# Kernel tuning notes

Hardware: AMD Instinct MI355X
Metric: run time of the kernel (lower is better)

## Reference

```python
import jax, jax.numpy as jnp
import numpy as np

N_USERS = 100000
N_ITEMS = 50000
N_ENT = 80000            # items + tags (tags = 30000)
N_NODES = N_USERS + N_ENT
N_EDGES = 800000
D = 64
N_LAYERS = 2


def _center_net(embs, idx, n, W1, b1, W2, b2):
    # CenterIntersection: linear+relu, linear, segment softmax, weighted segment sum
    act = jnp.maximum(embs @ W1.T + b1, 0.0)
    logits = act @ W2.T + b2
    m = jax.ops.segment_max(logits, idx, num_segments=n)
    e = jnp.exp(logits - m[idx])
    s = jax.ops.segment_sum(e, idx, num_segments=n)
    att = e / s[idx]
    return jax.ops.segment_sum(att * embs, idx, num_segments=n)


def _offset_net(embs, idx, mask, n, use_min, W1, b1, W2, b2):
    # BoxOffsetIntersection restricted to edges where mask is True
    mf = mask[:, None].astype(embs.dtype)
    act = jnp.maximum(embs @ W1.T + b1, 0.0) * mf
    cnt = jax.ops.segment_sum(mask.astype(embs.dtype), idx, num_segments=n)
    mean = jax.ops.segment_sum(act, idx, num_segments=n) / jnp.maximum(cnt, 1.0)[:, None]
    gate = jax.nn.sigmoid(mean @ W2.T + b2)
    if use_min:
        src = jnp.where(mask[:, None], embs, jnp.inf)
        red = jax.ops.segment_min(src, idx, num_segments=n)
    else:
        src = jnp.where(mask[:, None], embs, -jnp.inf)
        red = jax.ops.segment_max(src, idx, num_segments=n)
    red = jnp.where(jnp.isfinite(red), red, 0.0)  # torch_scatter fills empty segments with 0
    return red * gate


def setup_inputs() -> dict:
    key = jax.random.key(0)
    ks = jax.random.split(key, 10)
    s = 0.05  # xavier-like scale
    return {
        "user_emb": jax.random.normal(ks[0], (N_USERS, D), jnp.float32),
        "user_offset_emb": jax.random.normal(ks[1], (N_USERS, D), jnp.float32),
        "item_emb": jax.random.normal(ks[2], (N_ENT, D), jnp.float32),
        "item_offset_emb": jax.random.normal(ks[3], (N_ENT, D), jnp.float32),
        "cW1": jax.random.normal(ks[4], (D, D), jnp.float32) * s,
        "cb1": jnp.zeros((D,), jnp.float32),
        "cW2": jax.random.normal(ks[5], (D, D), jnp.float32) * s,
        "cb2": jnp.zeros((D,), jnp.float32),
        "oW1": jax.random.normal(ks[6], (D, D), jnp.float32) * s,
        "ob1": jnp.zeros((D,), jnp.float32),
        "oW2": jax.random.normal(ks[7], (D, D), jnp.float32) * s,
        "ob2": jnp.zeros((D,), jnp.float32),
        "head": jax.random.randint(ks[8], (N_EDGES,), 0, N_NODES, jnp.int32),
        "tail": jax.random.randint(ks[9], (N_EDGES,), 0, N_NODES, jnp.int32),
    }


def reference(user_emb, user_offset_emb, item_emb, item_offset_emb,
              cW1, cb1, cW2, cb2, oW1, ob1, oW2, ob2, head, tail):
    all_embs = jnp.concatenate([user_emb, item_emb], axis=0)              # [N_NODES, D]
    all_off = jnp.maximum(jnp.concatenate([user_offset_emb, item_offset_emb], axis=0), 0.0)
    uu_idx = jnp.concatenate([jnp.arange(N_USERS), jnp.arange(N_USERS)])
    uu_mask = jnp.ones((2 * N_USERS,), bool)
    m_inter = (tail >= N_USERS) & (head < N_USERS) & (tail < N_USERS + N_ITEMS)
    m_ut = (head < N_USERS) & (tail >= N_USERS + N_ITEMS)
    m_item = (head >= N_USERS) & (head < N_USERS + N_ITEMS)
    m_tag = head >= N_USERS + N_ITEMS
    for _ in range(N_LAYERS):
        h_embs = all_embs[tail]                                           # [E, D] gather
        agg_emb = _center_net(h_embs, head, N_NODES, cW1, cb1, cW2, cb2)
        edge_off = jnp.maximum(all_off[tail], 0.0)                        # [E, D]
        inter_u = _offset_net(edge_off, head, m_inter, N_NODES, True, oW1, ob1, oW2, ob2)[:N_USERS]
        ut_u = _offset_net(edge_off, head, m_ut, N_NODES, False, oW1, ob1, oW2, ob2)[:N_USERS]
        item_o = _offset_net(edge_off, head, m_item, N_NODES, False, oW1, ob1, oW2, ob2)[N_USERS:N_USERS + N_ITEMS]
        tag_o = _offset_net(edge_off, head, m_tag, N_NODES, True, oW1, ob1, oW2, ob2)[N_USERS + N_ITEMS:]
        uo_cat = jnp.concatenate([inter_u, ut_u], axis=0)                 # [2*N_USERS, D]
        user_o = jnp.maximum(_offset_net(uo_cat, uu_idx, uu_mask, N_USERS, False, oW1, ob1, oW2, ob2), 0.0)
        agg_off = jnp.concatenate([user_o, item_o, tag_o], axis=0)
        agg_emb = agg_emb / jnp.maximum(jnp.linalg.norm(agg_emb, axis=1, keepdims=True), 1e-12)  # F.normalize
        all_embs = agg_emb
        all_off = agg_off
    return (all_embs[:N_USERS], all_off[:N_USERS], all_embs[N_USERS:], all_off[N_USERS:])
```

## Files before the change

### kernel.cpp

```cpp
#include <hip/hip_runtime.h>
#include <hip/hip_fp16.h>
#include <math.h>

#define NU 100000
#define NI 50000
#define NENT 80000
#define NN 180000
#define NEDGE 800000
#define SCAN_NB ((NN + 1023) / 1024)
#define UFIN_BLKS ((NU + 63) / 64)
#define EFIN_BLKS (NENT / 64)

typedef _Float16 f16x4 __attribute__((ext_vector_type(4)));
typedef _Float16 f16x2 __attribute__((ext_vector_type(2)));
typedef float f32x4 __attribute__((ext_vector_type(4)));

__device__ __forceinline__ float sigmoid_f(float x) { return 1.0f / (1.0f + __expf(-x)); }
__device__ __forceinline__ unsigned pack2(float a, float b) {
    __half2 h = __floats2half2_rn(a, b);
    return *(unsigned*)&h;
}
__device__ __forceinline__ f16x2 u2h2(unsigned u) { union { unsigned u; f16x2 h; } x; x.u = u; return x.h; }
__device__ __forceinline__ float fdot2f(f16x2 a, f16x2 b, float c) {
#if __has_builtin(__builtin_amdgcn_fdot2)
    return __builtin_amdgcn_fdot2(a, b, c, false);
#else
    return (float)a[0] * (float)b[0] + (float)a[1] * (float)b[1] + c;
#endif
}
__device__ __forceinline__ _Float16 hminf(_Float16 a, _Float16 b) { return a < b ? a : b; }
__device__ __forceinline__ _Float16 hmaxf(_Float16 a, _Float16 b) { return a > b ? a : b; }

template<typename T>
__device__ __forceinline__ f16x4 ldfrag(const T* __restrict__ p) {
    if constexpr (sizeof(T) == 2) {
        return *(const f16x4*)p;
    } else {
        float4 v = *(const float4*)p;
        f16x4 r; r[0] = (_Float16)v.x; r[1] = (_Float16)v.y; r[2] = (_Float16)v.z; r[3] = (_Float16)v.w;
        return r;
    }
}
template<typename T>
__device__ __forceinline__ f16x4 ldfragr(const T* __restrict__ p) {
    if constexpr (sizeof(T) == 2) {
        f16x4 v = *(const f16x4*)p;
        #pragma unroll
        for (int i = 0; i < 4; ++i) v[i] = hmaxf(v[i], (_Float16)0.f);
        return v;
    } else {
        float4 v = *(const float4*)p;
        f16x4 r;
        r[0] = (_Float16)fmaxf(v.x, 0.f); r[1] = (_Float16)fmaxf(v.y, 0.f);
        r[2] = (_Float16)fmaxf(v.z, 0.f); r[3] = (_Float16)fmaxf(v.w, 0.f);
        return r;
    }
}
__device__ __forceinline__ f16x4 fragp(const _Float16* __restrict__ Wp, int dt, int ks, int lane) {
    return *(const f16x4*)(Wp + (((dt * 4 + ks) * 64 + lane) << 2));
}
__device__ __forceinline__ f32x4 mm(f16x4 a, f16x4 b, f32x4 c) {
    return __builtin_amdgcn_mfma_f32_16x16x16f16(a, b, c, 0, 0, 0);
}

__global__ __launch_bounds__(256) void prep_w(
    const float* __restrict__ W0, const float* __restrict__ W1,
    const float* __restrict__ W2, const float* __restrict__ W3,
    _Float16* __restrict__ out)
{
    int idx = blockIdx.x * 256 + threadIdx.x;
    int mat = idx >> 12, wi = idx & 4095;
    const float* W = (mat == 0) ? W0 : (mat == 1) ? W1 : (mat == 2) ? W2 : W3;
    int tile = wi >> 8;
    int dt = tile >> 2, ks = tile & 3;
    int ln = (wi >> 2) & 63, j = wi & 3;
    int lr = ln & 15, lk = ln >> 4;
    out[idx] = (_Float16)W[(size_t)(dt * 16 + lr) * 64 + ks * 16 + lk * 4 + j];
}

template<typename T>
__global__ __launch_bounds__(256) void node_pass(
    const T* __restrict__ embU, const T* __restrict__ embE,
    const T* __restrict__ offU, const T* __restrict__ offE,
    const _Float16* __restrict__ cW1f, const float* __restrict__ cb1,
    const _Float16* __restrict__ cW2f, const float* __restrict__ cb2,
    const _Float16* __restrict__ oW1f, const float* __restrict__ ob1,
    unsigned* __restrict__ packedA, unsigned* __restrict__ packedB)
{
    __shared__ _Float16 tb[4][16 * 72];
    int lane = threadIdx.x & 63, wid = threadIdx.x >> 6;
    int n0 = (blockIdx.x * 4 + wid) * 16;
    if (n0 >= NN) return;
    int lr = lane & 15, lk = lane >> 4;
    const T* eb; const T* ob;
    if (n0 < NU) { eb = embU + (size_t)n0 * 64; ob = offU + (size_t)n0 * 64; }
    else         { eb = embE + (size_t)(n0 - NU) * 64; ob = offE + (size_t)(n0 - NU) * 64; }

    f16x4 ax[4];
    #pragma unroll
    for (int ks = 0; ks < 4; ++ks) ax[ks] = ldfrag(eb + (size_t)lr * 64 + ks * 16 + lk * 4);
    f32x4 acc[4];
    #pragma unroll
    for (int dt = 0; dt < 4; ++dt) {
        float b = cb1[dt * 16 + lr];
        f32x4 c = {b, b, b, b};
        #pragma unroll
        for (int ks = 0; ks < 4; ++ks) c = mm(ax[ks], fragp(cW1f, dt, ks, lane), c);
        acc[dt] = c;
    }
    _Float16* T16 = tb[wid];
    #pragma unroll
    for (int dt = 0; dt < 4; ++dt)
        #pragma unroll
        for (int r = 0; r < 4; ++r)
            T16[(lk * 4 + r) * 72 + dt * 16 + lr] = (_Float16)fmaxf(acc[dt][r], 0.f);
    f16x4 a1[4];
    #pragma unroll
    for (int ks = 0; ks < 4; ++ks) a1[ks] = *(const f16x4*)(T16 + lr * 72 + ks * 16 + lk * 4);
    #pragma unroll
    for (int dt = 0; dt < 4; ++dt) {
        float b = cb2[dt * 16 + lr];
        f32x4 c = {b, b, b, b};
        #pragma unroll
        for (int ks = 0; ks < 4; ++ks) c = mm(a1[ks], fragp(cW2f, dt, ks, lane), c);
        acc[dt] = c;
    }
    f16x4 axo[4];
    #pragma unroll
    for (int ks = 0; ks < 4; ++ks) axo[ks] = ldfragr(ob + (size_t)lr * 64 + ks * 16 + lk * 4);
    f32x4 acco[4];
    #pragma unroll
    for (int dt = 0; dt < 4; ++dt) {
        float b = ob1[dt * 16 + lr];
        f32x4 c = {b, b, b, b};
        #pragma unroll
        for (int ks = 0; ks < 4; ++ks) c = mm(axo[ks], fragp(oW1f, dt, ks, lane), c);
        acco[dt] = c;
    }
    #pragma unroll
    for (int ks = 0; ks < 4; ++ks) *(f16x4*)(T16 + lr * 72 + ks * 16 + lk * 4) = ax[ks];
    _Float16 xv[16];
    #pragma unroll
    for (int dt = 0; dt < 4; ++dt)
        #pragma unroll
        for (int r = 0; r < 4; ++r) xv[dt * 4 + r] = T16[(lk * 4 + r) * 72 + dt * 16 + lr];
    #pragma unroll
    for (int ks = 0; ks < 4; ++ks) *(f16x4*)(T16 + lr * 72 + ks * 16 + lk * 4) = axo[ks];
    #pragma unroll
    for (int dt = 0; dt < 4; ++dt) {
        #pragma unroll
        for (int r = 0; r < 4; ++r) {
            int li = lk * 4 + r;
            float ev = __expf(acc[dt][r]);
            float xf = (float)xv[dt * 4 + r];
            float ovf = (float)T16[(lk * 4 + r) * 72 + dt * 16 + lr];
            float aov = fmaxf(acco[dt][r], 0.f);
            size_t idx = (size_t)(n0 + li) * 64 + dt * 16 + lr;
            packedA[idx] = pack2(ev, ev * xf);
            packedB[idx] = pack2(aov, ovf);
        }
    }
}

__global__ __launch_bounds__(256) void hist_k(const int* __restrict__ head, int* __restrict__ counts) {
    int e = blockIdx.x * 256 + threadIdx.x;
    if (e < NEDGE) atomicAdd(&counts[head[e]], 1);
}

__global__ __launch_bounds__(1024) void scan_local(const int* __restrict__ counts,
                                                   int* __restrict__ excl, int* __restrict__ partials) {
    __shared__ int wsum[16];
    int tid = threadIdx.x, lane = tid & 63, wid = tid >> 6;
    int i = blockIdx.x * 1024 + tid;
    int v = (i < NN) ? counts[i] : 0;
    int s = v;
    #pragma unroll
    for (int d = 1; d < 64; d <<= 1) { int u = __shfl_up(s, d, 64); if (lane >= d) s += u; }
    if (lane == 63) wsum[wid] = s;
    __syncthreads();
    if (wid == 0 && lane < 16) {
        int w = wsum[lane];
        #pragma unroll
        for (int d = 1; d < 16; d <<= 1) { int u = __shfl_up(w, d, 64); if (lane >= d) w += u; }
        wsum[lane] = w;
    }
    __syncthreads();
    int base = wid ? wsum[wid - 1] : 0;
    if (i < NN) excl[i] = base + s - v;
    if (tid == 1023) partials[blockIdx.x] = wsum[15];
}

__global__ __launch_bounds__(256) void scan_carry(const int* __restrict__ partials, int* __restrict__ carries) {
    __shared__ int ws[4];
    int tid = threadIdx.x, lane = tid & 63, wid = tid >> 6;
    int v = (tid < SCAN_NB) ? partials[tid] : 0;
    int s = v;
    #pragma unroll
    for (int d = 1; d < 64; d <<= 1) { int u = __shfl_up(s, d, 64); if (lane >= d) s += u; }
    if (lane == 63) ws[wid] = s;
    __syncthreads();
    int add = 0;
    for (int w = 0; w < wid; ++w) add += ws[w];
    if (tid < SCAN_NB) carries[tid] = add + s - v;
}

__global__ __launch_bounds__(1024) void scan_add(int* __restrict__ excl, const int* __restrict__ carries,
                                                 int* __restrict__ cursor) {
    int i = blockIdx.x * 1024 + threadIdx.x;
    if (i < NN) { int o = excl[i] + carries[blockIdx.x]; excl[i] = o; cursor[i] = o; }
    if (i == 0) excl[NN] = NEDGE;
}

__global__ __launch_bounds__(256) void scatter_k(const int* __restrict__ head, const int* __restrict__ tail,
                                                 int* __restrict__ cursor, int* __restrict__ sorted_t) {
    int e = blockIdx.x * 256 + threadIdx.x;
    if (e < NEDGE) { int pos = atomicAdd(&cursor[head[e]], 1); sorted_t[pos] = tail[e]; }
}

template<bool OUT16>
__global__ __launch_bounds__(256) void seg_pass(
    const unsigned* __restrict__ packedA, const unsigned* __restrict__ packedB,
    const int* __restrict__ offsets, const int* __restrict__ sorted_t,
    void* __restrict__ embOutU_, void* __restrict__ embOutE_,
    _Float16* __restrict__ meanI, _Float16* __restrict__ redI,
    _Float16* __restrict__ meanU, _Float16* __restrict__ redU,
    _Float16* __restrict__ meanE, _Float16* __restrict__ redE)
{
    int lane = threadIdx.x & 63;
    int h = blockIdx.x * 4 + (threadIdx.x >> 6);
    int beg = offsets[h], end = offsets[h + 1];
    bool isUser = (h < NU);
    bool entMin = (h >= NU + NI);
    const f16x2 SEL_LO = {(_Float16)1.0f, (_Float16)0.0f};
    const f16x2 SEL_HI = {(_Float16)0.0f, (_Float16)1.0f};
    float num = 0.f, den = 0.f, s_i = 0.f, s_u = 0.f;
    const _Float16 HINF = u2h2(0x7C007C00u)[0];
    _Float16 m_i = (isUser || entMin) ? HINF : (_Float16)0.f;
    _Float16 m_u = (_Float16)0.f;
    int c_i = 0, c_u = 0;

    const char* pA = (const char*)packedA;
    const char* pB = (const char*)packedB;
    int loff = lane << 2;

#define LOADQ(t, a, b)                                                          \
    do {                                                                        \
        a = *(const unsigned*)(pA + ((size_t)(unsigned)(t) << 8) + loff);       \
        if (!isUser || (t) >= NU)                                               \
            b = *(const unsigned*)(pB + ((size_t)(unsigned)(t) << 8) + loff);   \
    } while (0)

#define CONSUME(tc, qa, qb)                                                     \
    do {                                                                        \
        f16x2 ea = u2h2(qa);                                                    \
        den = fdot2f(ea, SEL_LO, den);                                          \
        num = fdot2f(ea, SEL_HI, num);                                          \
        if (isUser) {                                                           \
            if ((tc) >= NU) {                                                   \
                f16x2 ab = u2h2(qb);                                            \
                if ((tc) < NU + NI) { s_i = fdot2f(ab, SEL_LO, s_i); m_i = hminf(m_i, ab[1]); c_i++; } \
                else                { s_u = fdot2f(ab, SEL_LO, s_u); m_u = hmaxf(m_u, ab[1]); c_u++; } \
            }                                                                   \
        } else {                                                                \
            f16x2 ab = u2h2(qb);                                                \
            s_i = fdot2f(ab, SEL_LO, s_i); c_i++;                               \
            m_i = entMin ? hminf(m_i, ab[1]) : hmaxf(m_i, ab[1]);               \
        }                                                                       \
    } while (0)

    for (int base = beg; base < end; base += 64) {
        int rem = end - base; if (rem > 64) rem = 64;
        int tv = sorted_t[base + (lane < rem ? lane : 0)];
        int tA = 0, tB = 0; unsigned aA = 0, aB = 0, bA = 0, bB = 0;
        tA = __builtin_amdgcn_readlane(tv, 0);
        LOADQ(tA, aA, bA);
        if (rem > 1) { tB = __builtin_amdgcn_readlane(tv, 1); LOADQ(tB, aB, bB); }
        int j = 0;
        for (; j + 2 <= rem; j += 2) {
            CONSUME(tA, aA, bA);
            if (j + 2 < rem) { tA = __builtin_amdgcn_readlane(tv, j + 2); LOADQ(tA, aA, bA); }
            CONSUME(tB, aB, bB);
            if (j + 3 < rem) { tB = __builtin_amdgcn_readlane(tv, j + 3); LOADQ(tB, aB, bB); }
        }
        if (j < rem) CONSUME(tA, aA, bA);
    }
#undef LOADQ
#undef CONSUME

    float v = (den > 0.f) ? num / den : 0.f;
    float sq = v * v;
    #pragma unroll
    for (int m = 32; m; m >>= 1) sq += __shfl_xor(sq, m, 64);
    v = v / fmaxf(sqrtf(sq), 1e-12f);

    float m_if = (float)m_i;
    if (m_if > 1e37f) m_if = 0.f;
    float rc_i = __builtin_amdgcn_rcpf(fmaxf((float)c_i, 1.f));
    if (isUser) {
        size_t r = (size_t)h * 64 + lane;
        if constexpr (OUT16) ((_Float16*)embOutU_)[r] = (_Float16)v;
        else                 ((float*)embOutU_)[r] = v;
        float rc_u = __builtin_amdgcn_rcpf(fmaxf((float)c_u, 1.f));
        meanI[r] = (_Float16)(s_i * rc_i);
        redI[r]  = (_Float16)m_if;
        meanU[r] = (_Float16)(s_u * rc_u);
        redU[r]  = m_u;
    } else {
        size_t r = (size_t)(h - NU) * 64 + lane;
        if constexpr (OUT16) ((_Float16*)embOutE_)[r] = (_Float16)v;
        else                 ((float*)embOutE_)[r] = v;
        meanE[r] = (_Float16)(s_i * rc_i);
        redE[r]  = (_Float16)m_if;
    }
}

template<bool OUT16>
__global__ __launch_bounds__(256) void fin_pass(
    const _Float16* __restrict__ meanI, const _Float16* __restrict__ redI,
    const _Float16* __restrict__ meanU, const _Float16* __restrict__ redU,
    const _Float16* __restrict__ meanE, const _Float16* __restrict__ redE,
    const _Float16* __restrict__ oW1f, const float* __restrict__ ob1,
    const _Float16* __restrict__ oW2f, const float* __restrict__ ob2,
    void* __restrict__ outOffU_, void* __restrict__ entOff_)
{
    int lane = threadIdx.x & 63, wid = threadIdx.x >> 6;
    int lr = lane & 15, lk = lane >> 4;

    if (blockIdx.x >= UFIN_BLKS) {
        int n0 = (((int)blockIdx.x - UFIN_BLKS) * 4 + wid) * 16;
        if (n0 >= NENT) return;
        f16x4 am[4];
        #pragma unroll
        for (int ks = 0; ks < 4; ++ks) am[ks] = *(const f16x4*)(meanE + (size_t)(n0 + lr) * 64 + ks * 16 + lk * 4);
        #pragma unroll
        for (int dt = 0; dt < 4; ++dt) {
            float b = ob2[dt * 16 + lr];
            f32x4 c = {b, b, b, b};
            #pragma unroll
            for (int ks = 0; ks < 4; ++ks) c = mm(am[ks], fragp(oW2f, dt, ks, lane), c);
            #pragma unroll
            for (int r = 0; r < 4; ++r) {
                size_t row = (size_t)(n0 + lk * 4 + r);
                float val = (float)redE[row * 64 + dt * 16 + lr] * sigmoid_f(c[r]);
                if constexpr (OUT16) ((_Float16*)entOff_)[row * 64 + dt * 16 + lr] = (_Float16)val;
                else                 ((float*)entOff_)[row * 64 + dt * 16 + lr] = val;
            }
        }
        return;
    }

    __shared__ _Float16 tb[4][16 * 72];
    int u0 = (blockIdx.x * 4 + wid) * 16;
    if (u0 >= NU) return;
    _Float16* T16 = tb[wid];

    f16x4 W1f[4][4], W2f[4][4];
    float b1d[4], b2d[4];
    #pragma unroll
    for (int dt = 0; dt < 4; ++dt) {
        b1d[dt] = ob1[dt * 16 + lr]; b2d[dt] = ob2[dt * 16 + lr];
        #pragma unroll
        for (int ks = 0; ks < 4; ++ks) {
            W1f[dt][ks] = fragp(oW1f, dt, ks, lane);
            W2f[dt][ks] = fragp(oW2f, dt, ks, lane);
        }
    }

    f16x4 am[4];
    #pragma unroll
    for (int ks = 0; ks < 4; ++ks) am[ks] = *(const f16x4*)(meanI + (size_t)(u0 + lr) * 64 + ks * 16 + lk * 4);
    f32x4 iu[4], uu[4];
    #pragma unroll
    for (int dt = 0; dt < 4; ++dt) {
        f32x4 c = {b2d[dt], b2d[dt], b2d[dt], b2d[dt]};
        #pragma unroll
        for (int ks = 0; ks < 4; ++ks) c = mm(am[ks], W2f[dt][ks], c);
        #pragma unroll
        for (int r = 0; r < 4; ++r)
            iu[dt][r] = (float)redI[(size_t)(u0 + lk * 4 + r) * 64 + dt * 16 + lr] * sigmoid_f(c[r]);
    }
    #pragma unroll
    for (int ks = 0; ks < 4; ++ks) am[ks] = *(const f16x4*)(meanU + (size_t)(u0 + lr) * 64 + ks * 16 + lk * 4);
    #pragma unroll
    for (int dt = 0; dt < 4; ++dt) {
        f32x4 c = {b2d[dt], b2d[dt], b2d[dt], b2d[dt]};
        #pragma unroll
        for (int ks = 0; ks < 4; ++ks) c = mm(am[ks], W2f[dt][ks], c);
        #pragma unroll
        for (int r = 0; r < 4; ++r)
            uu[dt][r] = (float)redU[(size_t)(u0 + lk * 4 + r) * 64 + dt * 16 + lr] * sigmoid_f(c[r]);
    }
    #pragma unroll
    for (int dt = 0; dt < 4; ++dt)
        #pragma unroll
        for (int r = 0; r < 4; ++r) T16[(lk * 4 + r) * 72 + dt * 16 + lr] = (_Float16)iu[dt][r];
    #pragma unroll
    for (int ks = 0; ks < 4; ++ks) am[ks] = *(const f16x4*)(T16 + lr * 72 + ks * 16 + lk * 4);
    f32x4 mn[4];
    #pragma unroll
    for (int dt = 0; dt < 4; ++dt) {
        f32x4 c = {b1d[dt], b1d[dt], b1d[dt], b1d[dt]};
        #pragma unroll
        for (int ks = 0; ks < 4; ++ks) c = mm(am[ks], W1f[dt][ks], c);
        #pragma unroll
        for (int r = 0; r < 4; ++r) mn[dt][r] = fmaxf(c[r], 0.f);
    }
    #pragma unroll
    for (int dt = 0; dt < 4; ++dt)
        #pragma unroll
        for (int r = 0; r < 4; ++r) T16[(lk * 4 + r) * 72 + dt * 16 + lr] = (_Float16)uu[dt][r];
    #pragma unroll
    for (int ks = 0; ks < 4; ++ks) am[ks] = *(const f16x4*)(T16 + lr * 72 + ks * 16 + lk * 4);
    #pragma unroll
    for (int dt = 0; dt < 4; ++dt) {
        f32x4 c = {b1d[dt], b1d[dt], b1d[dt], b1d[dt]};
        #pragma unroll
        for (int ks = 0; ks < 4; ++ks) c = mm(am[ks], W1f[dt][ks], c);
        #pragma unroll
        for (int r = 0; r < 4; ++r) mn[dt][r] = 0.5f * (mn[dt][r] + fmaxf(c[r], 0.f));
    }
    #pragma unroll
    for (int dt = 0; dt < 4; ++dt)
        #pragma unroll
        for (int r = 0; r < 4; ++r) T16[(lk * 4 + r) * 72 + dt * 16 + lr] = (_Float16)mn[dt][r];
    #pragma unroll
    for (int ks = 0; ks < 4; ++ks) am[ks] = *(const f16x4*)(T16 + lr * 72 + ks * 16 + lk * 4);
    #pragma unroll
    for (int dt = 0; dt < 4; ++dt) {
        f32x4 c = {b2d[dt], b2d[dt], b2d[dt], b2d[dt]};
        #pragma unroll
        for (int ks = 0; ks < 4; ++ks) c = mm(am[ks], W2f[dt][ks], c);
        #pragma unroll
        for (int r = 0; r < 4; ++r) {
            float val = fmaxf(fmaxf(iu[dt][r], uu[dt][r]) * sigmoid_f(c[r]), 0.f);
            size_t idx = (size_t)(u0 + lk * 4 + r) * 64 + dt * 16 + lr;
            if constexpr (OUT16) ((_Float16*)outOffU_)[idx] = (_Float16)val;
            else                 ((float*)outOffU_)[idx] = val;
        }
    }
}

extern "C" void kernel_launch(void* const* d_in, const int* in_sizes, int n_in,
                              void* d_out, int out_size, void* d_ws, size_t ws_size,
                              hipStream_t stream)
{
    const float* user_emb = (const float*)d_in[0];
    const float* user_off = (const float*)d_in[1];
    const float* item_emb = (const float*)d_in[2];
    const float* item_off = (const float*)d_in[3];
    const float* cW1 = (const float*)d_in[4];
    const float* cb1 = (const float*)d_in[5];
    const float* cW2 = (const float*)d_in[6];
    const float* cb2 = (const float*)d_in[7];
    const float* oW1 = (const float*)d_in[8];
    const float* ob1 = (const float*)d_in[9];
    const float* oW2 = (const float*)d_in[10];
    const float* ob2 = (const float*)d_in[11];
    const int* head = (const int*)d_in[12];
    const int* tail = (const int*)d_in[13];
    float* out = (float*)d_out;

    const size_t SZ = (size_t)NN * 64;
    _Float16* A16   = (_Float16*)d_ws;
    _Float16* B16   = A16 + SZ;
    unsigned* packedA = (unsigned*)(B16 + SZ);
    unsigned* packedB = packedA + SZ;
    _Float16* meanI_h = (_Float16*)(packedB + SZ);
    _Float16* redI_h  = meanI_h + (size_t)NU * 64;
    _Float16* meanU_h = redI_h + (size_t)NU * 64;
    _Float16* redU_h  = meanU_h + (size_t)NU * 64;
    _Float16* meanE_h = redU_h + (size_t)NU * 64;
    _Float16* redE_h  = meanE_h + (size_t)NENT * 64;
    _Float16* wpre    = redE_h + (size_t)NENT * 64;
    int* counts   = (int*)(wpre + 4 * 4096);
    int* offsets  = counts + NN;
    int* cursor   = offsets + NN + 1;
    int* sorted_t = cursor + NN;
    int* partials = sorted_t + NEDGE;
    int* carries  = partials + SCAN_NB;

    const _Float16* cW1f = wpre;
    const _Float16* cW2f = wpre + 4096;
    const _Float16* oW1f = wpre + 8192;
    const _Float16* oW2f = wpre + 12288;

    prep_w<<<64, 256, 0, stream>>>(cW1, cW2, oW1, oW2, wpre);
    hipMemsetAsync(counts, 0, NN * sizeof(int), stream);
    hist_k<<<(NEDGE + 255) / 256, 256, 0, stream>>>(head, counts);
    scan_local<<<SCAN_NB, 1024, 0, stream>>>(counts, offsets, partials);
    scan_carry<<<1, 256, 0, stream>>>(partials, carries);
    scan_add<<<SCAN_NB, 1024, 0, stream>>>(offsets, carries, cursor);
    scatter_k<<<(NEDGE + 255) / 256, 256, 0, stream>>>(head, tail, cursor, sorted_t);

    node_pass<float><<<(NN + 63) / 64, 256, 0, stream>>>(
        user_emb, item_emb, user_off, item_off,
        cW1f, cb1, cW2f, cb2, oW1f, ob1, packedA, packedB);
    seg_pass<true><<<NN / 4, 256, 0, stream>>>(
        packedA, packedB, offsets, sorted_t,
        A16, A16 + (size_t)NU * 64,
        meanI_h, redI_h, meanU_h, redU_h, meanE_h, redE_h);
    fin_pass<true><<<UFIN_BLKS + EFIN_BLKS, 256, 0, stream>>>(
        meanI_h, redI_h, meanU_h, redU_h, meanE_h, redE_h,
        oW1f, ob1, oW2f, ob2, B16, B16 + (size_t)NU * 64);

    node_pass<_Float16><<<(NN + 63) / 64, 256, 0, stream>>>(
        A16, A16 + (size_t)NU * 64, B16, B16 + (size_t)NU * 64,
        cW1f, cb1, cW2f, cb2, oW1f, ob1, packedA, packedB);
    seg_pass<false><<<NN / 4, 256, 0, stream>>>(
        packedA, packedB, offsets, sorted_t,
        out, out + (size_t)2 * NU * 64,
        meanI_h, redI_h, meanU_h, redU_h, meanE_h, redE_h);
    fin_pass<false><<<UFIN_BLKS + EFIN_BLKS, 256, 0, stream>>>(
        meanI_h, redI_h, meanU_h, redU_h, meanE_h, redE_h,
        oW1f, ob1, oW2f, ob2, out + (size_t)NU * 64, out + ((size_t)2 * NU + NENT) * 64);
}
```

Measured before the change: 404.4 us.

## Swap MFMA operands to drop LDS transposes, vectorize stores, fuse histogram into node pass

Swaps the MFMA operand order so the weight fragment is the A operand and the activations the B operand. The output then lands in the layout the next layer's input expects, so node_pass and fin_pass no longer need LDS round-trips to transpose between chained matmuls. Outputs are now written as 16-byte vector stores, and biases are loaded as float4. The edge histogram kernel is folded into the first node_pass launch as extra blocks, which removes one launch and lets the atomics overlap with the MLP work; this requires node_pass to run before the scan.

```diff
diff --git a/kernel.cpp b/kernel.cpp
--- a/kernel.cpp
+++ b/kernel.cpp
@@ -10,6 +10,8 @@
 #define SCAN_NB ((NN + 1023) / 1024)
 #define UFIN_BLKS ((NU + 63) / 64)
 #define EFIN_BLKS (NENT / 64)
+#define NODE_BLKS ((NN / 16 + 3) / 4)
+#define HIST_BLKS ((NEDGE + 255) / 256)
 
 typedef _Float16 f16x4 __attribute__((ext_vector_type(4)));
 typedef _Float16 f16x2 __attribute__((ext_vector_type(2)));
@@ -59,8 +61,13 @@
 __device__ __forceinline__ f16x4 fragp(const _Float16* __restrict__ Wp, int dt, int ks, int lane) {
     return *(const f16x4*)(Wp + (((dt * 4 + ks) * 64 + lane) << 2));
 }
-__device__ __forceinline__ f32x4 mm(f16x4 a, f16x4 b, f32x4 c) {
-    return __builtin_amdgcn_mfma_f32_16x16x16f16(a, b, c, 0, 0, 0);
+__device__ __forceinline__ f32x4 mmw(f16x4 wfrag, f16x4 xfrag, f32x4 c) {
+    return __builtin_amdgcn_mfma_f32_16x16x16f16(wfrag, xfrag, c, 0, 0, 0);
+}
+__device__ __forceinline__ f32x4 bias4(const float* __restrict__ b, int dt, int lk) {
+    float4 v = *(const float4*)(b + dt * 16 + lk * 4);
+    f32x4 r = {v.x, v.y, v.z, v.w};
+    return r;
 }
 
 __global__ __launch_bounds__(256) void prep_w(
@@ -78,16 +85,21 @@
     out[idx] = (_Float16)W[(size_t)(dt * 16 + lr) * 64 + ks * 16 + lk * 4 + j];
 }
 
-template<typename T>
+template<typename T, bool HIST>
 __global__ __launch_bounds__(256) void node_pass(
     const T* __restrict__ embU, const T* __restrict__ embE,
     const T* __restrict__ offU, const T* __restrict__ offE,
     const _Float16* __restrict__ cW1f, const float* __restrict__ cb1,
     const _Float16* __restrict__ cW2f, const float* __restrict__ cb2,
     const _Float16* __restrict__ oW1f, const float* __restrict__ ob1,
-    unsigned* __restrict__ packedA, unsigned* __restrict__ packedB)
+    unsigned* __restrict__ packedA, unsigned* __restrict__ packedB,
+    const int* __restrict__ head, int* __restrict__ counts)
 {
-    __shared__ _Float16 tb[4][16 * 72];
+    if (HIST && blockIdx.x >= NODE_BLKS) {
+        int e = ((int)blockIdx.x - NODE_BLKS) * 256 + threadIdx.x;
+        if (e < NEDGE) atomicAdd(&counts[head[e]], 1);
+        return;
+    }
     int lane = threadIdx.x & 63, wid = threadIdx.x >> 6;
     int n0 = (blockIdx.x * 4 + wid) * 16;
     if (n0 >= NN) return;
@@ -96,75 +108,55 @@
     if (n0 < NU) { eb = embU + (size_t)n0 * 64; ob = offU + (size_t)n0 * 64; }
     else         { eb = embE + (size_t)(n0 - NU) * 64; ob = offE + (size_t)(n0 - NU) * 64; }
 
-    f16x4 ax[4];
-    #pragma unroll
-    for (int ks = 0; ks < 4; ++ks) ax[ks] = ldfrag(eb + (size_t)lr * 64 + ks * 16 + lk * 4);
-    f32x4 acc[4];
-    #pragma unroll
-    for (int dt = 0; dt < 4; ++dt) {
-        float b = cb1[dt * 16 + lr];
-        f32x4 c = {b, b, b, b};
-        #pragma unroll
-        for (int ks = 0; ks < 4; ++ks) c = mm(ax[ks], fragp(cW1f, dt, ks, lane), c);
-        acc[dt] = c;
-    }
-    _Float16* T16 = tb[wid];
-    #pragma unroll
-    for (int dt = 0; dt < 4; ++dt)
-        #pragma unroll
-        for (int r = 0; r < 4; ++r)
-            T16[(lk * 4 + r) * 72 + dt * 16 + lr] = (_Float16)fmaxf(acc[dt][r], 0.f);
-    f16x4 a1[4];
-    #pragma unroll
-    for (int ks = 0; ks < 4; ++ks) a1[ks] = *(const f16x4*)(T16 + lr * 72 + ks * 16 + lk * 4);
-    #pragma unroll
-    for (int dt = 0; dt < 4; ++dt) {
-        float b = cb2[dt * 16 + lr];
-        f32x4 c = {b, b, b, b};
-        #pragma unroll
-        for (int ks = 0; ks < 4; ++ks) c = mm(a1[ks], fragp(cW2f, dt, ks, lane), c);
-        acc[dt] = c;
-    }
-    f16x4 axo[4];
-    #pragma unroll
-    for (int ks = 0; ks < 4; ++ks) axo[ks] = ldfragr(ob + (size_t)lr * 64 + ks * 16 + lk * 4);
-    f32x4 acco[4];
-    #pragma unroll
-    for (int dt = 0; dt < 4; ++dt) {
-        float b = ob1[dt * 16 + lr];
-        f32x4 c = {b, b, b, b};
-        #pragma unroll
-        for (int ks = 0; ks < 4; ++ks) c = mm(axo[ks], fragp(oW1f, dt, ks, lane), c);
-        acco[dt] = c;
-    }
-    #pragma unroll
-    for (int ks = 0; ks < 4; ++ks) *(f16x4*)(T16 + lr * 72 + ks * 16 + lk * 4) = ax[ks];
-    _Float16 xv[16];
-    #pragma unroll
-    for (int dt = 0; dt < 4; ++dt)
-        #pragma unroll
-        for (int r = 0; r < 4; ++r) xv[dt * 4 + r] = T16[(lk * 4 + r) * 72 + dt * 16 + lr];
-    #pragma unroll
-    for (int ks = 0; ks < 4; ++ks) *(f16x4*)(T16 + lr * 72 + ks * 16 + lk * 4) = axo[ks];
-    #pragma unroll
-    for (int dt = 0; dt < 4; ++dt) {
+    f16x4 ax[4], axo[4];
+    #pragma unroll
+    for (int ks = 0; ks < 4; ++ks) {
+        ax[ks]  = ldfrag(eb + (size_t)lr * 64 + ks * 16 + lk * 4);
+        axo[ks] = ldfragr(ob + (size_t)lr * 64 + ks * 16 + lk * 4);
+    }
+    f32x4 a1c[4];
+    #pragma unroll
+    for (int dt = 0; dt < 4; ++dt) {
+        f32x4 c = bias4(cb1, dt, lk);
+        #pragma unroll
+        for (int ks = 0; ks < 4; ++ks) c = mmw(fragp(cW1f, dt, ks, lane), ax[ks], c);
+        a1c[dt] = c;
+    }
+    f16x4 a1f[4];
+    #pragma unroll
+    for (int ks = 0; ks < 4; ++ks)
+        #pragma unroll
+        for (int r = 0; r < 4; ++r) a1f[ks][r] = (_Float16)fmaxf(a1c[ks][r], 0.f);
+    f32x4 lg[4];
+    #pragma unroll
+    for (int dt = 0; dt < 4; ++dt) {
+        f32x4 c = bias4(cb2, dt, lk);
+        #pragma unroll
+        for (int ks = 0; ks < 4; ++ks) c = mmw(fragp(cW2f, dt, ks, lane), a1f[ks], c);
+        lg[dt] = c;
+    }
+    f32x4 ao[4];
+    #pragma unroll
+    for (int dt = 0; dt < 4; ++dt) {
+        f32x4 c = bias4(ob1, dt, lk);
+        #pragma unroll
+        for (int ks = 0; ks < 4; ++ks) c = mmw(fragp(oW1f, dt, ks, lane), axo[ks], c);
+        ao[dt] = c;
+    }
+    #pragma unroll
+    for (int dt = 0; dt < 4; ++dt) {
+        uint4 ua, ub;
+        unsigned* pa = &ua.x; unsigned* pb = &ub.x;
         #pragma unroll
         for (int r = 0; r < 4; ++r) {
-            int li = lk * 4 + r;
-            float ev = __expf(acc[dt][r]);
-            float xf = (float)xv[dt * 4 + r];
-            float ovf = (float)T16[(lk * 4 + r) * 72 + dt * 16 + lr];
-            float aov = fmaxf(acco[dt][r], 0.f);
-            size_t idx = (size_t)(n0 + li) * 64 + dt * 16 + lr;
-            packedA[idx] = pack2(ev, ev * xf);
-            packedB[idx] = pack2(aov, ovf);
+            float ev = __expf(lg[dt][r]);
+            pa[r] = pack2(ev, ev * (float)ax[dt][r]);
+            pb[r] = pack2(fmaxf(ao[dt][r], 0.f), (float)axo[dt][r]);
         }
-    }
-}
-
-__global__ __launch_bounds__(256) void hist_k(const int* __restrict__ head, int* __restrict__ counts) {
-    int e = blockIdx.x * 256 + threadIdx.x;
-    if (e < NEDGE) atomicAdd(&counts[head[e]], 1);
+        size_t idx = (size_t)(n0 + lr) * 64 + dt * 16 + lk * 4;
+        *(uint4*)(packedA + idx) = ua;
+        *(uint4*)(packedB + idx) = ub;
+    }
 }
 
 __global__ __launch_bounds__(1024) void scan_local(const int* __restrict__ counts,
@@ -334,108 +326,109 @@
         for (int ks = 0; ks < 4; ++ks) am[ks] = *(const f16x4*)(meanE + (size_t)(n0 + lr) * 64 + ks * 16 + lk * 4);
         #pragma unroll
         for (int dt = 0; dt < 4; ++dt) {
-            float b = ob2[dt * 16 + lr];
-            f32x4 c = {b, b, b, b};
+            f32x4 c = bias4(ob2, dt, lk);
             #pragma unroll
-            for (int ks = 0; ks < 4; ++ks) c = mm(am[ks], fragp(oW2f, dt, ks, lane), c);
-            #pragma unroll
-            for (int r = 0; r < 4; ++r) {
-                size_t row = (size_t)(n0 + lk * 4 + r);
-                float val = (float)redE[row * 64 + dt * 16 + lr] * sigmoid_f(c[r]);
-                if constexpr (OUT16) ((_Float16*)entOff_)[row * 64 + dt * 16 + lr] = (_Float16)val;
-                else                 ((float*)entOff_)[row * 64 + dt * 16 + lr] = val;
+            for (int ks = 0; ks < 4; ++ks) c = mmw(fragp(oW2f, dt, ks, lane), am[ks], c);
+            size_t idx = (size_t)(n0 + lr) * 64 + dt * 16 + lk * 4;
+            f16x4 red = *(const f16x4*)(redE + idx);
+            if constexpr (OUT16) {
+                f16x4 o;
+                #pragma unroll
+                for (int r = 0; r < 4; ++r) o[r] = (_Float16)((float)red[r] * sigmoid_f(c[r]));
+                *(f16x4*)((_Float16*)entOff_ + idx) = o;
+            } else {
+                float4 o;
+                float* po = &o.x;
+                #pragma unroll
+                for (int r = 0; r < 4; ++r) po[r] = (float)red[r] * sigmoid_f(c[r]);
+                *(float4*)((float*)entOff_ + idx) = o;
             }
         }
         return;
     }
 
-    __shared__ _Float16 tb[4][16 * 72];
     int u0 = (blockIdx.x * 4 + wid) * 16;
     if (u0 >= NU) return;
-    _Float16* T16 = tb[wid];
 
     f16x4 W1f[4][4], W2f[4][4];
-    float b1d[4], b2d[4];
-    #pragma unroll
-    for (int dt = 0; dt < 4; ++dt) {
-        b1d[dt] = ob1[dt * 16 + lr]; b2d[dt] = ob2[dt * 16 + lr];
+    #pragma unroll
+    for (int dt = 0; dt < 4; ++dt)
         #pragma unroll
         for (int ks = 0; ks < 4; ++ks) {
             W1f[dt][ks] = fragp(oW1f, dt, ks, lane);
             W2f[dt][ks] = fragp(oW2f, dt, ks, lane);
         }
-    }
 
     f16x4 am[4];
+    f32x4 iu[4], uu[4];
     #pragma unroll
     for (int ks = 0; ks < 4; ++ks) am[ks] = *(const f16x4*)(meanI + (size_t)(u0 + lr) * 64 + ks * 16 + lk * 4);
-    f32x4 iu[4], uu[4];
-    #pragma unroll
-    for (int dt = 0; dt < 4; ++dt) {
-        f32x4 c = {b2d[dt], b2d[dt], b2d[dt], b2d[dt]};
-        #pragma unroll
-        for (int ks = 0; ks < 4; ++ks) c = mm(am[ks], W2f[dt][ks], c);
-        #pragma unroll
-        for (int r = 0; r < 4; ++r)
-            iu[dt][r] = (float)redI[(size_t)(u0 + lk * 4 + r) * 64 + dt * 16 + lr] * sigmoid_f(c[r]);
+    #pragma unroll
+    for (int dt = 0; dt < 4; ++dt) {
+        f32x4 c = bias4(ob2, dt, lk);
+        #pragma unroll
+        for (int ks = 0; ks < 4; ++ks) c = mmw(W2f[dt][ks], am[ks], c);
+        f16x4 red = *(const f16x4*)(redI + (size_t)(u0 + lr) * 64 + dt * 16 + lk * 4);
+        #pragma unroll
+        for (int r = 0; r < 4; ++r) iu[dt][r] = (float)red[r] * sigmoid_f(c[r]);
     }
     #pragma unroll
     for (int ks = 0; ks < 4; ++ks) am[ks] = *(const f16x4*)(meanU + (size_t)(u0 + lr) * 64 + ks * 16 + lk * 4);
     #pragma unroll
     for (int dt = 0; dt < 4; ++dt) {
-        f32x4 c = {b2d[dt], b2d[dt], b2d[dt], b2d[dt]};
-        #pragma unroll
-        for (int ks = 0; ks < 4; ++ks) c = mm(am[ks], W2f[dt][ks], c);
-        #pragma unroll
-        for (int r = 0; r < 4; ++r)
-            uu[dt][r] = (float)redU[(size_t)(u0 + lk * 4 + r) * 64 + dt * 16 + lr] * sigmoid_f(c[r]);
-    }
-    #pragma unroll
-    for (int dt = 0; dt < 4; ++dt)
-        #pragma unroll
-        for (int r = 0; r < 4; ++r) T16[(lk * 4 + r) * 72 + dt * 16 + lr] = (_Float16)iu[dt][r];
-    #pragma unroll
-    for (int ks = 0; ks < 4; ++ks) am[ks] = *(const f16x4*)(T16 + lr * 72 + ks * 16 + lk * 4);
+        f32x4 c = bias4(ob2, dt, lk);
+        #pragma unroll
+        for (int ks = 0; ks < 4; ++ks) c = mmw(W2f[dt][ks], am[ks], c);
+        f16x4 red = *(const f16x4*)(redU + (size_t)(u0 + lr) * 64 + dt * 16 + lk * 4);
+        #pragma unroll
+        for (int r = 0; r < 4; ++r) uu[dt][r] = (float)red[r] * sigmoid_f(c[r]);
+    }
+    f16x4 iuf[4], uuf[4];
+    #pragma unroll
+    for (int ks = 0; ks < 4; ++ks)
+        #pragma unroll
+        for (int r = 0; r < 4; ++r) { iuf[ks][r] = (_Float16)iu[ks][r]; uuf[ks][r] = (_Float16)uu[ks][r]; }
     f32x4 mn[4];
     #pragma unroll
     for (int dt = 0; dt < 4; ++dt) {
-        f32x4 c = {b1d[dt], b1d[dt], b1d[dt], b1d[dt]};
-        #pragma unroll
-        for (int ks = 0; ks < 4; ++ks) c = mm(am[ks], W1f[dt][ks], c);
+        f32x4 c = bias4(ob1, dt, lk);
+        #pragma unroll
+        for (int ks = 0; ks < 4; ++ks) c = mmw(W1f[dt][ks], iuf[ks], c);
         #pragma unroll
         for (int r = 0; r < 4; ++r) mn[dt][r] = fmaxf(c[r], 0.f);
     }
     #pragma unroll
-    for (int dt = 0; dt < 4; ++dt)
-        #pragma unroll
-        for (int r = 0; r < 4; ++r) T16[(lk * 4 + r) * 72 + dt * 16 + lr] = (_Float16)uu[dt][r];
-    #pragma unroll
-    for (int ks = 0; ks < 4; ++ks) am[ks] = *(const f16x4*)(T16 + lr * 72 + ks * 16 + lk * 4);
-    #pragma unroll
-    for (int dt = 0; dt < 4; ++dt) {
-        f32x4 c = {b1d[dt], b1d[dt], b1d[dt], b1d[dt]};
-        #pragma unroll
-        for (int ks = 0; ks < 4; ++ks) c = mm(am[ks], W1f[dt][ks], c);
+    for (int dt = 0; dt < 4; ++dt) {
+        f32x4 c = bias4(ob1, dt, lk);
+        #pragma unroll
+        for (int ks = 0; ks < 4; ++ks) c = mmw(W1f[dt][ks], uuf[ks], c);
         #pragma unroll
         for (int r = 0; r < 4; ++r) mn[dt][r] = 0.5f * (mn[dt][r] + fmaxf(c[r], 0.f));
     }
-    #pragma unroll
-    for (int dt = 0; dt < 4; ++dt)
-        #pragma unroll
-        for (int r = 0; r < 4; ++r) T16[(lk * 4 + r) * 72 + dt * 16 + lr] = (_Float16)mn[dt][r];
-    #pragma unroll
-    for (int ks = 0; ks < 4; ++ks) am[ks] = *(const f16x4*)(T16 + lr * 72 + ks * 16 + lk * 4);
-    #pragma unroll
-    for (int dt = 0; dt < 4; ++dt) {
-        f32x4 c = {b2d[dt], b2d[dt], b2d[dt], b2d[dt]};
-        #pragma unroll
-        for (int ks = 0; ks < 4; ++ks) c = mm(am[ks], W2f[dt][ks], c);
-        #pragma unroll
-        for (int r = 0; r < 4; ++r) {
-            float val = fmaxf(fmaxf(iu[dt][r], uu[dt][r]) * sigmoid_f(c[r]), 0.f);
-            size_t idx = (size_t)(u0 + lk * 4 + r) * 64 + dt * 16 + lr;
-            if constexpr (OUT16) ((_Float16*)outOffU_)[idx] = (_Float16)val;
-            else                 ((float*)outOffU_)[idx] = val;
+    f16x4 mnf[4];
+    #pragma unroll
+    for (int ks = 0; ks < 4; ++ks)
+        #pragma unroll
+        for (int r = 0; r < 4; ++r) mnf[ks][r] = (_Float16)mn[ks][r];
+    #pragma unroll
+    for (int dt = 0; dt < 4; ++dt) {
+        f32x4 c = bias4(ob2, dt, lk);
+        #pragma unroll
+        for (int ks = 0; ks < 4; ++ks) c = mmw(W2f[dt][ks], mnf[ks], c);
+        size_t idx = (size_t)(u0 + lr) * 64 + dt * 16 + lk * 4;
+        if constexpr (OUT16) {
+            f16x4 o;
+            #pragma unroll
+            for (int r = 0; r < 4; ++r)
+                o[r] = (_Float16)fmaxf(fmaxf(iu[dt][r], uu[dt][r]) * sigmoid_f(c[r]), 0.f);
+            *(f16x4*)((_Float16*)outOffU_ + idx) = o;
+        } else {
+            float4 o;
+            float* po = &o.x;
+            #pragma unroll
+            for (int r = 0; r < 4; ++r)
+                po[r] = fmaxf(fmaxf(iu[dt][r], uu[dt][r]) * sigmoid_f(c[r]), 0.f);
+            *(float4*)((float*)outOffU_ + idx) = o;
         }
     }
 }
@@ -486,15 +479,16 @@
 
     prep_w<<<64, 256, 0, stream>>>(cW1, cW2, oW1, oW2, wpre);
     hipMemsetAsync(counts, 0, NN * sizeof(int), stream);
-    hist_k<<<(NEDGE + 255) / 256, 256, 0, stream>>>(head, counts);
+
+    node_pass<float, true><<<NODE_BLKS + HIST_BLKS, 256, 0, stream>>>(
+        user_emb, item_emb, user_off, item_off,
+        cW1f, cb1, cW2f, cb2, oW1f, ob1, packedA, packedB, head, counts);
+
     scan_local<<<SCAN_NB, 1024, 0, stream>>>(counts, offsets, partials);
     scan_carry<<<1, 256, 0, stream>>>(partials, carries);
     scan_add<<<SCAN_NB, 1024, 0, stream>>>(offsets, carries, cursor);
     scatter_k<<<(NEDGE + 255) / 256, 256, 0, stream>>>(head, tail, cursor, sorted_t);
 
-    node_pass<float><<<(NN + 63) / 64, 256, 0, stream>>>(
-        user_emb, item_emb, user_off, item_off,
-        cW1f, cb1, cW2f, cb2, oW1f, ob1, packedA, packedB);
     seg_pass<true><<<NN / 4, 256, 0, stream>>>(
         packedA, packedB, offsets, sorted_t,
         A16, A16 + (size_t)NU * 64,
@@ -503,9 +497,9 @@
         meanI_h, redI_h, meanU_h, redU_h, meanE_h, redE_h,
         oW1f, ob1, oW2f, ob2, B16, B16 + (size_t)NU * 64);
 
-    node_pass<_Float16><<<(NN + 63) / 64, 256, 0, stream>>>(
+    node_pass<_Float16, false><<<NODE_BLKS, 256, 0, stream>>>(
         A16, A16 + (size_t)NU * 64, B16, B16 + (size_t)NU * 64,
-        cW1f, cb1, cW2f, cb2, oW1f, ob1, packedA, packedB);
+        cW1f, cb1, cW2f, cb2, oW1f, ob1, packedA, packedB, head, counts);
     seg_pass<false><<<NN / 4, 256, 0, stream>>>(
         packedA, packedB, offsets, sorted_t,
         out, out + (size_t)2 * NU * 64,
```

Measured after the change: 408.9 us. Within noise of the previous version (+1.1%).
